# Kernel optimization log

Hardware: AMD Instinct MI355X
Metric: run time of the kernel (lower is better)

Reference implementation:

```python
import jax, jax.numpy as jnp
import numpy as np

NEG = -9e15  # matches torch's -9000000000000000.0 masking constant


def setup_inputs() -> dict:
    key = jax.random.key(0)
    kq, kk, kv, ka = jax.random.split(key, 4)
    B, H, N, d = 8, 8, 1024, 128
    queries = jax.random.normal(kq, (B, H, N, d), dtype=jnp.float32)
    keys = jax.random.normal(kk, (B, H, N, d), dtype=jnp.float32)
    values = jax.random.normal(kv, (B, H, N, d), dtype=jnp.float32)
    adj = jax.random.randint(ka, (N, N), 0, 2, dtype=jnp.int32)
    return {"queries": queries, "keys": keys, "values": values, "adj": adj}


def reference(queries, keys, values, adj):
    # scores: [B,H,N,N]; original divides by the constant 8 (not sqrt(dim))
    e = jnp.einsum("bhnd,bhmd->bhnm", queries, keys) / 8.0
    # adjacency mask [N,N] broadcasts over batch and heads
    att = jnp.where(adj > 0, e, jnp.asarray(NEG, e.dtype))
    att = jax.nn.softmax(att, axis=-1)
    # dropout is identity in eval mode
    h = jnp.einsum("bhnm,bhmd->bhnd", att, values)  # [B,H,N,d]
    B, H, N, d = h.shape
    # original uses .view (raw reshape), NOT a permute
    return jnp.reshape(h, (N, B, H, d))
```

## Files before the change

### kernel.cpp

```cpp
#include <hip/hip_runtime.h>
#include <hip/hip_bf16.h>


typedef __bf16 bf16x8 __attribute__((ext_vector_type(8)));
typedef float  f32x4  __attribute__((ext_vector_type(4)));

#define NSEQ 1024
#define DH   128
#define BM   64
#define BN   64
#define NKT  (NSEQ / BN)
#define KS_STRIDE 136
#define VT_STRIDE 64
#define PS_STRIDE 72
#define SHIFT 8.0f

__device__ __forceinline__ float f4get(const float4& v, int c) {
    return (c == 0) ? v.x : (c == 1) ? v.y : (c == 2) ? v.z : v.w;
}

__global__ __launch_bounds__(256, 4)
void graph_attn_kernel(const float* __restrict__ Q,
                       const float* __restrict__ K,
                       const float* __restrict__ V,
                       const int*   __restrict__ adj,
                       float*       __restrict__ out)
{
    __shared__ __attribute__((aligned(16))) __bf16 KsP[BN * KS_STRIDE];
    __shared__ __attribute__((aligned(16))) __bf16 Vt [DH * VT_STRIDE];

    const int tid  = threadIdx.x;
    const int wave = tid >> 6;
    const int lane = tid & 63;
    const int n16  = lane & 15;
    const int quad = lane >> 4;

    const int id   = blockIdx.x;
    const int bh   = (id & 7) * 8 + ((id >> 3) & 7);
    const int qt   = id >> 6;
    const int q0   = qt * BM;
    const size_t base = (size_t)bh * NSEQ * DH;

    const int rp   = tid >> 4;
    const int kcol = (tid & 15) * 8;
    const int db   = tid & 31;
    const int kvb  = tid >> 5;

    bf16x8 qf[4];
    #pragma unroll
    for (int ks = 0; ks < 4; ++ks) {
        const float* src = Q + base + (size_t)(q0 + wave * 16 + n16) * DH + ks * 32 + quad * 8;
        float4 a = *(const float4*)(src);
        float4 b = *(const float4*)(src + 4);
        bf16x8 w;
        w[0] = (__bf16)a.x; w[1] = (__bf16)a.y; w[2] = (__bf16)a.z; w[3] = (__bf16)a.w;
        w[4] = (__bf16)b.x; w[5] = (__bf16)b.y; w[6] = (__bf16)b.z; w[7] = (__bf16)b.w;
        qf[ks] = w;
    }

    f32x4 o[8];
    #pragma unroll
    for (int i = 0; i < 8; ++i) o[i] = (f32x4){0.f, 0.f, 0.f, 0.f};
    float lp[4] = {0.f, 0.f, 0.f, 0.f};
    const int qrow = q0 + wave * 16 + quad * 4;

    for (int kt = 0; kt < NKT; ++kt) {
        const int kv0 = kt * BN;
        __syncthreads();

        #pragma unroll
        for (int it = 0; it < 4; ++it) {
            int row = 16 * it + rp;
            const float* src = K + base + (size_t)(kv0 + row) * DH + kcol;
            float4 a = *(const float4*)(src);
            float4 b = *(const float4*)(src + 4);
            bf16x8 w;
            w[0] = (__bf16)a.x; w[1] = (__bf16)a.y; w[2] = (__bf16)a.z; w[3] = (__bf16)a.w;
            w[4] = (__bf16)b.x; w[5] = (__bf16)b.y; w[6] = (__bf16)b.z; w[7] = (__bf16)b.w;
            *(bf16x8*)(&KsP[row * KS_STRIDE + kcol]) = w;
        }
        {
            float4 vreg[8];
            #pragma unroll
            for (int rr = 0; rr < 8; ++rr)
                vreg[rr] = *(const float4*)(V + base + (size_t)(kv0 + kvb * 8 + rr) * DH + db * 4);
            #pragma unroll
            for (int c = 0; c < 4; ++c) {
                bf16x8 w;
                #pragma unroll
                for (int j = 0; j < 8; ++j) w[j] = (__bf16)f4get(vreg[j], c);
                int d = db * 4 + c;
                int s = (d ^ (d >> 3)) & 7;
                *(bf16x8*)(&Vt[d * VT_STRIDE + ((kvb ^ s) << 3)]) = w;
            }
        }
        __syncthreads();

        int am[4][4];
        #pragma unroll
        for (int i = 0; i < 4; ++i)
            #pragma unroll
            for (int t = 0; t < 4; ++t)
                am[i][t] = adj[(size_t)(qrow + i) * NSEQ + kv0 + t * 16 + n16];

        float sc[4][4];
        #pragma unroll
        for (int t = 0; t < 4; ++t) {
            f32x4 acc = (f32x4){0.f, 0.f, 0.f, 0.f};
            #pragma unroll
            for (int ks = 0; ks < 4; ++ks) {
                bf16x8 bfr = *(const bf16x8*)(&KsP[(t * 16 + n16) * KS_STRIDE + ks * 32 + quad * 8]);
                acc = __builtin_amdgcn_mfma_f32_16x16x32_bf16(qf[ks], bfr, acc, 0, 0, 0);
            }
            #pragma unroll
            for (int i = 0; i < 4; ++i) sc[t][i] = acc[i];
        }
        __syncthreads();

        #pragma unroll
        for (int i = 0; i < 4; ++i) {
            const int prow = wave * 16 + quad * 4 + i;
            float rowsum = 0.f;
            #pragma unroll
            for (int t = 0; t < 4; ++t) {
                float p = __expf(sc[t][i] * 0.125f - SHIFT);
                p = (am[i][t] > 0) ? p : 0.f;
                rowsum += p;
                KsP[prow * PS_STRIDE + t * 16 + n16] = (__bf16)p;
            }
            lp[i] += rowsum;
        }

        #pragma unroll
        for (int ks = 0; ks < 2; ++ks) {
            bf16x8 pf = *(const bf16x8*)(&KsP[(wave * 16 + n16) * PS_STRIDE + ks * 32 + quad * 8]);
            #pragma unroll
            for (int nt = 0; nt < 8; ++nt) {
                int d = nt * 16 + n16;
                int s = (d ^ (d >> 3)) & 7;
                int kvbr = ks * 4 + quad;
                bf16x8 vf = *(const bf16x8*)(&Vt[d * VT_STRIDE + ((kvbr ^ s) << 3)]);
                o[nt] = __builtin_amdgcn_mfma_f32_16x16x32_bf16(pf, vf, o[nt], 0, 0, 0);
            }
        }
    }

    float linv[4];
    #pragma unroll
    for (int i = 0; i < 4; ++i) {
        float ls = lp[i];
        ls += __shfl_xor(ls, 1);
        ls += __shfl_xor(ls, 2);
        ls += __shfl_xor(ls, 4);
        ls += __shfl_xor(ls, 8);
        linv[i] = 1.0f / fmaxf(ls, 1e-30f);
    }
    #pragma unroll
    for (int nt = 0; nt < 8; ++nt)
        #pragma unroll
        for (int i = 0; i < 4; ++i)
            out[base + (size_t)(qrow + i) * DH + nt * 16 + n16] = o[nt][i] * linv[i];
}

extern "C" void kernel_launch(void* const* d_in, const int* in_sizes, int n_in,
                              void* d_out, int out_size, void* d_ws, size_t ws_size,
                              hipStream_t stream) {
    const float* Q   = (const float*)d_in[0];
    const float* K   = (const float*)d_in[1];
    const float* V   = (const float*)d_in[2];
    const int*   adj = (const int*)d_in[3];
    float* out = (float*)d_out;
    graph_attn_kernel<<<1024, 256, 0, stream>>>(Q, K, V, adj, out);
}
```

Before: 206.9 us.

## Prepack K/V to bf16 tiles and stream them via global_load_lds

Adds a prepack kernel that converts K and V to bf16 once, writing them into swizzled per-tile layouts in the workspace. The main attention kernel then copies each tile directly into LDS with global_load_lds and processes 128 query rows per block (two 16-row tiles per wave), so each K/V tile is reused across twice as many queries. This removes the repeated fp32 load and convert work for K/V, which the old kernel did in every query-tile block. It also drops one barrier by using a separate P buffer and switches the exp to exp2 with folded constants. The cost is an extra kernel launch, workspace traffic and lower occupancy (launch bounds 2), and a fallback path covers the case where the workspace is too small.

```diff
diff --git a/kernel.cpp b/kernel.cpp
--- a/kernel.cpp
+++ b/kernel.cpp
@@ -4,79 +4,252 @@
 
 typedef __bf16 bf16x8 __attribute__((ext_vector_type(8)));
 typedef float  f32x4  __attribute__((ext_vector_type(4)));
+typedef unsigned int u32;
 
 #define NSEQ 1024
 #define DH   128
-#define BM   64
 #define BN   64
-#define NKT  (NSEQ / BN)
-#define KS_STRIDE 136
-#define VT_STRIDE 64
-#define PS_STRIDE 72
-#define SHIFT 8.0f
+#define NKT  16
+#define TILE_ELEMS (BN * DH)
+#define C1 0.1803368801111244f
+#define C2 11.5415603271110070f
 
 __device__ __forceinline__ float f4get(const float4& v, int c) {
     return (c == 0) ? v.x : (c == 1) ? v.y : (c == 2) ? v.z : v.w;
 }
 
-__global__ __launch_bounds__(256, 4)
-void graph_attn_kernel(const float* __restrict__ Q,
-                       const float* __restrict__ K,
-                       const float* __restrict__ V,
-                       const int*   __restrict__ adj,
-                       float*       __restrict__ out)
+__device__ __forceinline__ void gload_lds16(const void* g, void* l) {
+    __builtin_amdgcn_global_load_lds(
+        (const __attribute__((address_space(1))) u32*)g,
+        (__attribute__((address_space(3))) u32*)l, 16, 0, 0);
+}
+
+__global__ __launch_bounds__(256)
+void prepack_kernel(const float* __restrict__ K, const float* __restrict__ V,
+                    __bf16* __restrict__ Kws, __bf16* __restrict__ Vws)
 {
-    __shared__ __attribute__((aligned(16))) __bf16 KsP[BN * KS_STRIDE];
-    __shared__ __attribute__((aligned(16))) __bf16 Vt [DH * VT_STRIDE];
+    const int tid = threadIdx.x;
+    const int id  = blockIdx.x;
+    const size_t gbase = (size_t)(id >> 4) * NSEQ * DH + (size_t)(id & 15) * BN * DH;
+    __bf16* ko = Kws + (size_t)id * TILE_ELEMS;
+    __bf16* vo = Vws + (size_t)id * TILE_ELEMS;
+
+    {
+        const int r  = tid >> 2;
+        const int c0 = (tid & 3) * 4;
+        #pragma unroll
+        for (int cc = 0; cc < 4; ++cc) {
+            const int c = c0 + cc;
+            const float* src = K + gbase + (size_t)r * DH + c * 8;
+            float4 a = *(const float4*)src;
+            float4 b = *(const float4*)(src + 4);
+            bf16x8 w;
+            w[0]=(__bf16)a.x; w[1]=(__bf16)a.y; w[2]=(__bf16)a.z; w[3]=(__bf16)a.w;
+            w[4]=(__bf16)b.x; w[5]=(__bf16)b.y; w[6]=(__bf16)b.z; w[7]=(__bf16)b.w;
+            const int cs = (c & 8) | ((c ^ (r & 7)) & 7);
+            *(bf16x8*)(ko + r * DH + cs * 8) = w;
+        }
+    }
+    {
+        const int vkvb = tid >> 5;
+        const int vdb  = tid & 31;
+        float4 vr[8];
+        #pragma unroll
+        for (int rr = 0; rr < 8; ++rr)
+            vr[rr] = *(const float4*)(V + gbase + (size_t)(vkvb * 8 + rr) * DH + vdb * 4);
+        #pragma unroll
+        for (int c = 0; c < 4; ++c) {
+            const int d = vdb * 4 + c;
+            bf16x8 w;
+            #pragma unroll
+            for (int j = 0; j < 8; ++j) w[j] = (__bf16)f4get(vr[j], c);
+            const int cs = vkvb ^ (d & 7);
+            *(bf16x8*)(vo + d * BN + cs * 8) = w;
+        }
+    }
+}
+
+__global__ __launch_bounds__(256, 2)
+void attn_fast(const float* __restrict__ Q, const __bf16* __restrict__ Kws,
+               const __bf16* __restrict__ Vws, const int* __restrict__ adj,
+               float* __restrict__ out)
+{
+    __shared__ __attribute__((aligned(16))) __bf16 Kt[TILE_ELEMS];
+    __shared__ __attribute__((aligned(16))) __bf16 Vt[TILE_ELEMS];
+    __shared__ __attribute__((aligned(16))) __bf16 Ps[128 * 72];
 
     const int tid  = threadIdx.x;
     const int wave = tid >> 6;
     const int lane = tid & 63;
     const int n16  = lane & 15;
     const int quad = lane >> 4;
-
-    const int id   = blockIdx.x;
-    const int bh   = (id & 7) * 8 + ((id >> 3) & 7);
-    const int qt   = id >> 6;
-    const int q0   = qt * BM;
+    const int m7   = n16 & 7;
+
+    const int id = blockIdx.x;
+    const int bh = (id & 7) * 8 + ((id >> 3) & 7);
+    const int q0 = (id >> 6) * 128;
+    const size_t base  = (size_t)bh * NSEQ * DH;
+    const size_t tile0 = (size_t)(bh * NKT) * TILE_ELEMS;
+
+    bf16x8 qf[2][4];
+    #pragma unroll
+    for (int rt = 0; rt < 2; ++rt)
+        #pragma unroll
+        for (int ks = 0; ks < 4; ++ks) {
+            const float* src = Q + base + (size_t)(q0 + wave * 32 + rt * 16 + n16) * DH
+                             + ks * 32 + quad * 8;
+            float4 a = *(const float4*)src;
+            float4 b = *(const float4*)(src + 4);
+            bf16x8 w;
+            w[0]=(__bf16)a.x; w[1]=(__bf16)a.y; w[2]=(__bf16)a.z; w[3]=(__bf16)a.w;
+            w[4]=(__bf16)b.x; w[5]=(__bf16)b.y; w[6]=(__bf16)b.z; w[7]=(__bf16)b.w;
+            qf[rt][ks] = w;
+        }
+
+    f32x4 o[2][8];
+    #pragma unroll
+    for (int rt = 0; rt < 2; ++rt)
+        #pragma unroll
+        for (int i = 0; i < 8; ++i) o[rt][i] = (f32x4){0.f, 0.f, 0.f, 0.f};
+    float lp[2][4] = {{0.f,0.f,0.f,0.f},{0.f,0.f,0.f,0.f}};
+
+    for (int kt = 0; kt < NKT; ++kt) {
+        const int kv0 = kt * BN;
+        __syncthreads();
+
+        const __bf16* ktile = Kws + tile0 + (size_t)kt * TILE_ELEMS;
+        const __bf16* vtile = Vws + tile0 + (size_t)kt * TILE_ELEMS;
+        #pragma unroll
+        for (int j = 0; j < 4; ++j) {
+            const int off = wave * 2048 + j * 512;
+            gload_lds16(ktile + off + lane * 8, &Kt[off]);
+            gload_lds16(vtile + off + lane * 8, &Vt[off]);
+        }
+        __syncthreads();
+
+        int am[2][4][4];
+        #pragma unroll
+        for (int rt = 0; rt < 2; ++rt)
+            #pragma unroll
+            for (int i = 0; i < 4; ++i)
+                #pragma unroll
+                for (int t = 0; t < 4; ++t)
+                    am[rt][i][t] = adj[(size_t)(q0 + wave * 32 + rt * 16 + quad * 4 + i) * NSEQ
+                                       + kv0 + t * 16 + n16];
+
+        float sc[2][4][4];
+        #pragma unroll
+        for (int t = 0; t < 4; ++t) {
+            f32x4 acc0 = (f32x4){0.f, 0.f, 0.f, 0.f};
+            f32x4 acc1 = (f32x4){0.f, 0.f, 0.f, 0.f};
+            #pragma unroll
+            for (int ks = 0; ks < 4; ++ks) {
+                const int c  = ks * 4 + quad;
+                const int cs = (c & 8) | ((c ^ m7) & 7);
+                bf16x8 bfr = *(const bf16x8*)(&Kt[(t * 16 + n16) * DH + cs * 8]);
+                acc0 = __builtin_amdgcn_mfma_f32_16x16x32_bf16(qf[0][ks], bfr, acc0, 0, 0, 0);
+                acc1 = __builtin_amdgcn_mfma_f32_16x16x32_bf16(qf[1][ks], bfr, acc1, 0, 0, 0);
+            }
+            #pragma unroll
+            for (int i = 0; i < 4; ++i) { sc[0][t][i] = acc0[i]; sc[1][t][i] = acc1[i]; }
+        }
+
+        #pragma unroll
+        for (int rt = 0; rt < 2; ++rt)
+            #pragma unroll
+            for (int i = 0; i < 4; ++i) {
+                const int prow = wave * 32 + rt * 16 + quad * 4 + i;
+                float rowsum = 0.f;
+                #pragma unroll
+                for (int t = 0; t < 4; ++t) {
+                    float p = exp2f(sc[rt][t][i] * C1 - C2);
+                    p = (am[rt][i][t] > 0) ? p : 0.f;
+                    rowsum += p;
+                    Ps[prow * 72 + t * 16 + n16] = (__bf16)p;
+                }
+                lp[rt][i] += rowsum;
+            }
+
+        #pragma unroll
+        for (int ks = 0; ks < 2; ++ks) {
+            bf16x8 pf0 = *(const bf16x8*)(&Ps[(wave * 32 + n16)      * 72 + ks * 32 + quad * 8]);
+            bf16x8 pf1 = *(const bf16x8*)(&Ps[(wave * 32 + 16 + n16) * 72 + ks * 32 + quad * 8]);
+            #pragma unroll
+            for (int nt = 0; nt < 8; ++nt) {
+                const int d  = nt * 16 + n16;
+                const int cs = (ks * 4 + quad) ^ m7;
+                bf16x8 vf = *(const bf16x8*)(&Vt[d * BN + cs * 8]);
+                o[0][nt] = __builtin_amdgcn_mfma_f32_16x16x32_bf16(pf0, vf, o[0][nt], 0, 0, 0);
+                o[1][nt] = __builtin_amdgcn_mfma_f32_16x16x32_bf16(pf1, vf, o[1][nt], 0, 0, 0);
+            }
+        }
+    }
+
+    #pragma unroll
+    for (int rt = 0; rt < 2; ++rt) {
+        float linv[4];
+        #pragma unroll
+        for (int i = 0; i < 4; ++i) {
+            float ls = lp[rt][i];
+            ls += __shfl_xor(ls, 1);
+            ls += __shfl_xor(ls, 2);
+            ls += __shfl_xor(ls, 4);
+            ls += __shfl_xor(ls, 8);
+            linv[i] = 1.0f / fmaxf(ls, 1e-30f);
+        }
+        const int qrow = q0 + wave * 32 + rt * 16 + quad * 4;
+        #pragma unroll
+        for (int nt = 0; nt < 8; ++nt)
+            #pragma unroll
+            for (int i = 0; i < 4; ++i)
+                out[base + (size_t)(qrow + i) * DH + nt * 16 + n16] = o[rt][nt][i] * linv[i];
+    }
+}
+
+#define KS_STRIDE 136
+#define VT_STRIDE 64
+#define PS_STRIDE 72
+
+__global__ __launch_bounds__(256, 4)
+void attn_fallback(const float* __restrict__ Q, const float* __restrict__ K,
+                   const float* __restrict__ V, const int* __restrict__ adj,
+                   float* __restrict__ out)
+{
+    __shared__ __attribute__((aligned(16))) __bf16 KsP[BN * KS_STRIDE];
+    __shared__ __attribute__((aligned(16))) __bf16 Vts[DH * VT_STRIDE];
+    const int tid = threadIdx.x;
+    const int wave = tid >> 6, lane = tid & 63, n16 = lane & 15, quad = lane >> 4;
+    const int id = blockIdx.x;
+    const int bh = (id & 7) * 8 + ((id >> 3) & 7);
+    const int q0 = (id >> 6) * 64;
     const size_t base = (size_t)bh * NSEQ * DH;
-
-    const int rp   = tid >> 4;
-    const int kcol = (tid & 15) * 8;
-    const int db   = tid & 31;
-    const int kvb  = tid >> 5;
-
+    const int rp = tid >> 4, kcol = (tid & 15) * 8, db = tid & 31, kvb = tid >> 5;
     bf16x8 qf[4];
     #pragma unroll
     for (int ks = 0; ks < 4; ++ks) {
         const float* src = Q + base + (size_t)(q0 + wave * 16 + n16) * DH + ks * 32 + quad * 8;
-        float4 a = *(const float4*)(src);
-        float4 b = *(const float4*)(src + 4);
+        float4 a = *(const float4*)src; float4 b = *(const float4*)(src + 4);
         bf16x8 w;
-        w[0] = (__bf16)a.x; w[1] = (__bf16)a.y; w[2] = (__bf16)a.z; w[3] = (__bf16)a.w;
-        w[4] = (__bf16)b.x; w[5] = (__bf16)b.y; w[6] = (__bf16)b.z; w[7] = (__bf16)b.w;
+        w[0]=(__bf16)a.x; w[1]=(__bf16)a.y; w[2]=(__bf16)a.z; w[3]=(__bf16)a.w;
+        w[4]=(__bf16)b.x; w[5]=(__bf16)b.y; w[6]=(__bf16)b.z; w[7]=(__bf16)b.w;
         qf[ks] = w;
     }
-
     f32x4 o[8];
     #pragma unroll
     for (int i = 0; i < 8; ++i) o[i] = (f32x4){0.f, 0.f, 0.f, 0.f};
     float lp[4] = {0.f, 0.f, 0.f, 0.f};
     const int qrow = q0 + wave * 16 + quad * 4;
-
     for (int kt = 0; kt < NKT; ++kt) {
         const int kv0 = kt * BN;
         __syncthreads();
-
         #pragma unroll
         for (int it = 0; it < 4; ++it) {
             int row = 16 * it + rp;
             const float* src = K + base + (size_t)(kv0 + row) * DH + kcol;
-            float4 a = *(const float4*)(src);
-            float4 b = *(const float4*)(src + 4);
+            float4 a = *(const float4*)src; float4 b = *(const float4*)(src + 4);
             bf16x8 w;
-            w[0] = (__bf16)a.x; w[1] = (__bf16)a.y; w[2] = (__bf16)a.z; w[3] = (__bf16)a.w;
-            w[4] = (__bf16)b.x; w[5] = (__bf16)b.y; w[6] = (__bf16)b.z; w[7] = (__bf16)b.w;
+            w[0]=(__bf16)a.x; w[1]=(__bf16)a.y; w[2]=(__bf16)a.z; w[3]=(__bf16)a.w;
+            w[4]=(__bf16)b.x; w[5]=(__bf16)b.y; w[6]=(__bf16)b.z; w[7]=(__bf16)b.w;
             *(bf16x8*)(&KsP[row * KS_STRIDE + kcol]) = w;
         }
         {
@@ -89,20 +262,17 @@
                 bf16x8 w;
                 #pragma unroll
                 for (int j = 0; j < 8; ++j) w[j] = (__bf16)f4get(vreg[j], c);
-                int d = db * 4 + c;
-                int s = (d ^ (d >> 3)) & 7;
-                *(bf16x8*)(&Vt[d * VT_STRIDE + ((kvb ^ s) << 3)]) = w;
-            }
-        }
-        __syncthreads();
-
+                int d = db * 4 + c, s = (d ^ (d >> 3)) & 7;
+                *(bf16x8*)(&Vts[d * VT_STRIDE + ((kvb ^ s) << 3)]) = w;
+            }
+        }
+        __syncthreads();
         int am[4][4];
         #pragma unroll
         for (int i = 0; i < 4; ++i)
             #pragma unroll
             for (int t = 0; t < 4; ++t)
                 am[i][t] = adj[(size_t)(qrow + i) * NSEQ + kv0 + t * 16 + n16];
-
         float sc[4][4];
         #pragma unroll
         for (int t = 0; t < 4; ++t) {
@@ -116,43 +286,36 @@
             for (int i = 0; i < 4; ++i) sc[t][i] = acc[i];
         }
         __syncthreads();
-
         #pragma unroll
         for (int i = 0; i < 4; ++i) {
             const int prow = wave * 16 + quad * 4 + i;
             float rowsum = 0.f;
             #pragma unroll
             for (int t = 0; t < 4; ++t) {
-                float p = __expf(sc[t][i] * 0.125f - SHIFT);
+                float p = exp2f(sc[t][i] * C1 - C2);
                 p = (am[i][t] > 0) ? p : 0.f;
                 rowsum += p;
                 KsP[prow * PS_STRIDE + t * 16 + n16] = (__bf16)p;
             }
             lp[i] += rowsum;
         }
-
         #pragma unroll
         for (int ks = 0; ks < 2; ++ks) {
             bf16x8 pf = *(const bf16x8*)(&KsP[(wave * 16 + n16) * PS_STRIDE + ks * 32 + quad * 8]);
             #pragma unroll
             for (int nt = 0; nt < 8; ++nt) {
-                int d = nt * 16 + n16;
-                int s = (d ^ (d >> 3)) & 7;
-                int kvbr = ks * 4 + quad;
-                bf16x8 vf = *(const bf16x8*)(&Vt[d * VT_STRIDE + ((kvbr ^ s) << 3)]);
+                int d = nt * 16 + n16, s = (d ^ (d >> 3)) & 7, kvbr = ks * 4 + quad;
+                bf16x8 vf = *(const bf16x8*)(&Vts[d * VT_STRIDE + ((kvbr ^ s) << 3)]);
                 o[nt] = __builtin_amdgcn_mfma_f32_16x16x32_bf16(pf, vf, o[nt], 0, 0, 0);
             }
         }
     }
-
     float linv[4];
     #pragma unroll
     for (int i = 0; i < 4; ++i) {
         float ls = lp[i];
-        ls += __shfl_xor(ls, 1);
-        ls += __shfl_xor(ls, 2);
-        ls += __shfl_xor(ls, 4);
-        ls += __shfl_xor(ls, 8);
+        ls += __shfl_xor(ls, 1); ls += __shfl_xor(ls, 2);
+        ls += __shfl_xor(ls, 4); ls += __shfl_xor(ls, 8);
         linv[i] = 1.0f / fmaxf(ls, 1e-30f);
     }
     #pragma unroll
@@ -170,5 +333,13 @@
     const float* V   = (const float*)d_in[2];
     const int*   adj = (const int*)d_in[3];
     float* out = (float*)d_out;
-    graph_attn_kernel<<<1024, 256, 0, stream>>>(Q, K, V, adj, out);
-}
+    const size_t need = (size_t)2 * 64 * NKT * TILE_ELEMS * sizeof(__bf16);
+    if (ws_size >= need) {
+        __bf16* Kws = (__bf16*)d_ws;
+        __bf16* Vws = Kws + (size_t)64 * NKT * TILE_ELEMS;
+        prepack_kernel<<<1024, 256, 0, stream>>>(K, V, Kws, Vws);
+        attn_fast<<<512, 256, 0, stream>>>(Q, Kws, Vws, adj, out);
+    } else {
+        attn_fallback<<<1024, 256, 0, stream>>>(Q, K, V, adj, out);
+    }
+}
```

Measured after the change: 197.8 us. -4.4%, faster.
